# Kernel optimization log

Hardware: AMD Instinct MI355X
Metric: run time of the kernel (lower is better)

Reference implementation:

```python
import jax, jax.numpy as jnp
import numpy as np
from math import factorial

IRREPS = [0] * 256 + [1] * 256 + [2] * 128 + [3] * 64
N_BATCH, CHANNELS = 1024, 32


def _dfact(n):
    r = 1
    while n > 1:
        r *= n
        n -= 2
    return r


def _sh_l(l, xyz):
    """Real spherical harmonics of degree l, components m=-l..l, at unit vectors xyz."""
    x, y, z = xyz[:, 0], xyz[:, 1], xyz[:, 2]
    phi = np.arctan2(y, x)
    ct = z
    st = np.sqrt(np.clip(1.0 - ct * ct, 0.0, None))
    Y = np.zeros((xyz.shape[0], 2 * l + 1))
    for m in range(l + 1):
        pmm = ((-1.0) ** m) * _dfact(2 * m - 1) * st ** m  # P_m^m(cos t)
        if l == m:
            plm = pmm
        else:
            pm1 = ct * (2 * m + 1) * pmm  # P_{m+1}^m
            if l == m + 1:
                plm = pm1
            else:
                p2, p1 = pmm, pm1
                for ll in range(m + 2, l + 1):
                    p2, p1 = p1, ((2 * ll - 1) * ct * p1 - (ll + m - 1) * p2) / (ll - m)
                plm = p1
        K = np.sqrt((2 * l + 1) / (4 * np.pi) * factorial(l - m) / factorial(l + m))
        if m == 0:
            Y[:, l] = K * plm
        else:
            Y[:, l + m] = np.sqrt(2.0) * K * np.cos(m * phi) * plm
            Y[:, l - m] = np.sqrt(2.0) * K * np.sin(m * phi) * plm
    return Y


def _j_matrix(l):
    """Orthogonal involution J_l: real-SH matrix of the y<->z axis swap (J = J^T = J^-1)."""
    rng = np.random.default_rng(0)
    v = rng.normal(size=(max(256, 16 * (2 * l + 1)), 3))
    v /= np.linalg.norm(v, axis=1, keepdims=True)
    A = _sh_l(l, v)
    B = _sh_l(l, v[:, [0, 2, 1]])  # Y(swap r)
    X, _, _, _ = np.linalg.lstsq(A, B, rcond=None)
    return X.T  # Y(swap r) = J @ Y(r)


def _build_info():
    freq, rev, groups = [], [], []
    off = 0
    i = 0
    while i < len(IRREPS):
        l = IRREPS[i]
        mul = 0
        while i < len(IRREPS) and IRREPS[i] == l:
            mul += 1
            i += 1
        d = 2 * l + 1
        groups.append((l, off, mul, np.asarray(_j_matrix(l), np.float32)))
        for _ in range(mul):
            for k in range(d):
                freq.append(k - l)      # m value of component k
                rev.append(off + (d - 1 - k))  # index of the -m partner
            off += d
    return np.asarray(freq, np.float32), np.asarray(rev, np.int32), groups, off


FREQ_NP, REV_NP, GROUPS, DIM = _build_info()
FREQ = jnp.asarray(FREQ_NP)
REV = jnp.asarray(REV_NP)
J_MATS = [jnp.asarray(J) for (_, _, _, J) in GROUPS]


def _z_rot(x, theta):
    """Per-m z-rotation (sparse vecsca): out_m = cos(m t) x_m - sin(m t) x_{-m}."""
    ang = theta[:, None] * FREQ  # (N, DIM)
    return jnp.cos(ang)[..., None] * x - jnp.sin(ang)[..., None] * x[:, REV, :]


def _j_apply(x):
    """Block-diagonal J application, grouped by l (sparse scale / flip stage)."""
    n, _, c = x.shape
    outs = []
    for (l, off, mul, _), J in zip(GROUPS, J_MATS):
        d = 2 * l + 1
        seg = x[:, off:off + mul * d, :].reshape(n, mul, d, c)
        outs.append(jnp.einsum('pq,nmqc->nmpc', J, seg).reshape(n, mul * d, c))
    return jnp.concatenate(outs, axis=1)


def setup_inputs() -> dict:
    key = jax.random.key(0)
    k0, k1, k2, k3 = jax.random.split(key, 4)
    two_pi = 2.0 * np.pi
    return {
        'input': jax.random.normal(k0, (N_BATCH, DIM, CHANNELS), dtype=jnp.float32),
        'alpha': jax.random.uniform(k1, (N_BATCH,), dtype=jnp.float32) * two_pi,
        'beta': jax.random.uniform(k2, (N_BATCH,), dtype=jnp.float32) * two_pi,
        'gamma': jax.random.uniform(k3, (N_BATCH,), dtype=jnp.float32) * two_pi,
    }


def reference(input, alpha, beta, gamma):
    # D(alpha, beta, gamma) = Dz(alpha) J Dz(beta) J Dz(gamma)
    x = _z_rot(input, gamma)
    x = _j_apply(x)
    x = _z_rot(x, beta)
    x = _j_apply(x)
    return _z_rot(x, alpha)
```

## Files before the change

kernel.cpp:

```cpp
#include <hip/hip_runtime.h>
#include <math.h>


namespace {

constexpr float SQ3_2 = 0.86602540378443864676f;
constexpr float S6    = 0.61237243569579452455f;
constexpr float S10   = 0.79056941504209483300f;
constexpr float S15   = 0.96824583655185422129f;

template<int L> struct JM;
template<> struct JM<1> {
  static constexpr float v[3][3] = {
    { 0.f, -1.f, 0.f},
    {-1.f,  0.f, 0.f},
    { 0.f,  0.f, 1.f}};
};
template<> struct JM<2> {
  static constexpr float v[5][5] = {
    { 0.f, 0.f,  0.f,   -1.f,  0.f},
    { 0.f, 1.f,  0.f,    0.f,  0.f},
    { 0.f, 0.f, -0.5f,   0.f, -SQ3_2},
    {-1.f, 0.f,  0.f,    0.f,  0.f},
    { 0.f, 0.f, -SQ3_2,  0.f,  0.5f}};
};
template<> struct JM<3> {
  static constexpr float v[7][7] = {
    { 0.f, 0.f, 0.f, S10,  0.f,   -S6,  0.f},
    { 0.f, 1.f, 0.f, 0.f,  0.f,    0.f, 0.f},
    { 0.f, 0.f, 0.f, S6,   0.f,    S10, 0.f},
    { S10, 0.f, S6,  0.f,  0.f,    0.f, 0.f},
    { 0.f, 0.f, 0.f, 0.f, -0.25f,  0.f, -S15},
    {-S6,  0.f, S10, 0.f,  0.f,    0.f, 0.f},
    { 0.f, 0.f, 0.f, 0.f, -S15,    0.f, 0.25f}};
};

template<int L>
__device__ inline void compute_M_col(int q, float al, float be, float ga, float* M) {
  constexpr int D = 2 * L + 1;
  const int mq = q - L;
  float sg, cg;
  sincosf((float)mq * ga, &sg, &cg);
  float v[D];
#pragma unroll
  for (int p = 0; p < D; ++p)
    v[p] = cg * JM<L>::v[p][q] + sg * JM<L>::v[p][(D - 1) - q];
  float c1, s1;
  sincosf(be, &s1, &c1);
  float cb[L + 1], sb[L + 1];
  cb[0] = 1.f; sb[0] = 0.f;
  cb[1] = c1;  sb[1] = s1;
#pragma unroll
  for (int k = 2; k <= L; ++k) {
    cb[k] = 2.f * c1 * cb[k - 1] - cb[k - 2];
    sb[k] = 2.f * c1 * sb[k - 1] - sb[k - 2];
  }
  float w[D];
#pragma unroll
  for (int p = 0; p < D; ++p) {
    const int mp = p - L;
    const int am = mp < 0 ? -mp : mp;
    const float c = cb[am];
    const float s = mp < 0 ? -sb[am] : sb[am];
    w[p] = c * v[p] - s * v[(D - 1) - p];
  }
  float u[D];
#pragma unroll
  for (int p = 0; p < D; ++p) {
    float acc = 0.f;
#pragma unroll
    for (int r = 0; r < D; ++r) acc = fmaf(JM<L>::v[p][r], w[r], acc);
    u[p] = acc;
  }
  sincosf(al, &s1, &c1);
  float ca[L + 1], sa[L + 1];
  ca[0] = 1.f; sa[0] = 0.f;
  ca[1] = c1;  sa[1] = s1;
#pragma unroll
  for (int k = 2; k <= L; ++k) {
    ca[k] = 2.f * c1 * ca[k - 1] - ca[k - 2];
    sa[k] = 2.f * c1 * sa[k - 1] - sa[k - 2];
  }
#pragma unroll
  for (int p = 0; p < D; ++p) {
    const int mp = p - L;
    const int am = mp < 0 ? -mp : mp;
    const float c = ca[am];
    const float s = mp < 0 ? -sa[am] : sa[am];
    M[p * D + q] = c * u[p] - s * u[(D - 1) - p];
  }
}

template<int D>
__device__ inline void apply_block(const float4* __restrict__ inN,
                                   float4* __restrict__ outN,
                                   const float* __restrict__ M, int off, int ch) {
  float4 v[D];
#pragma unroll
  for (int q = 0; q < D; ++q) v[q] = inN[(off + q) * 8 + ch];
#pragma unroll
  for (int p = 0; p < D; ++p) {
    float m = M[p * D];
    float4 a;
    a.x = m * v[0].x; a.y = m * v[0].y; a.z = m * v[0].z; a.w = m * v[0].w;
#pragma unroll
    for (int q = 1; q < D; ++q) {
      m = M[p * D + q];
      a.x = fmaf(m, v[q].x, a.x);
      a.y = fmaf(m, v[q].y, a.y);
      a.z = fmaf(m, v[q].z, a.z);
      a.w = fmaf(m, v[q].w, a.w);
    }
    outN[(off + p) * 8 + ch] = a;
  }
}

__global__ __launch_bounds__(256) void wigner_d_kernel(
    const float* __restrict__ in, const float* __restrict__ alpha,
    const float* __restrict__ beta, const float* __restrict__ gamma,
    float* __restrict__ out) {
  __shared__ float M1[9], M2[25], M3[49];
  const int n = blockIdx.x;
  const int t = threadIdx.x;

  if (t < 19) {
    const float al = alpha[n], be = beta[n], ga = gamma[n];
    if (t < 7)                  compute_M_col<3>(t,      al, be, ga, M3);
    else if (t >= 8 && t < 13)  compute_M_col<2>(t - 8,  al, be, ga, M2);
    else if (t >= 16)           compute_M_col<1>(t - 16, al, be, ga, M1);
  }
  __syncthreads();

  const size_t base = (size_t)n * (2112 * 8);
  const float4* inN = (const float4*)in + base;
  float4* outN = (float4*)out + base;
  const int g = t >> 3;
  const int ch = t & 7;

#pragma unroll
  for (int j = 0; j < 8; ++j) {
    const int r = 32 * j + g;
    outN[r * 8 + ch] = inN[r * 8 + ch];
  }
  for (int j = 0; j < 8; ++j)
    apply_block<3>(inN, outN, M1, 256 + 3 * (32 * j + g), ch);
  for (int j = 0; j < 4; ++j)
    apply_block<5>(inN, outN, M2, 1024 + 5 * (32 * j + g), ch);
  for (int j = 0; j < 2; ++j)
    apply_block<7>(inN, outN, M3, 1664 + 7 * (32 * j + g), ch);
}

}

extern "C" void kernel_launch(void* const* d_in, const int* in_sizes, int n_in,
                              void* d_out, int out_size, void* d_ws, size_t ws_size,
                              hipStream_t stream) {
  const float* in    = (const float*)d_in[0];
  const float* alpha = (const float*)d_in[1];
  const float* beta  = (const float*)d_in[2];
  const float* gamma = (const float*)d_in[3];
  float* out = (float*)d_out;
  const int n_batch = in_sizes[1];
  wigner_d_kernel<<<n_batch, 256, 0, stream>>>(in, alpha, beta, gamma, out);
}
```

Before: 115.9 us.

## Precompute Wigner matrices in separate kernel, widen blocks, use nontemporal IO

Moves the per-sample Wigner D matrix construction into a separate small kernel that writes to workspace. The streaming kernel then only loads the 83 coefficients into shared memory, so the serial trig prologue no longer stalls the whole block. Blocks grow to 512 threads with fully unrolled loops, and all global loads and stores use nontemporal hints. The cost is an extra kernel launch plus a workspace round trip, and a fused fallback is kept for when the workspace is too small.

```diff
diff --git a/kernel.cpp b/kernel.cpp
--- a/kernel.cpp
+++ b/kernel.cpp
@@ -3,6 +3,8 @@
 
 
 namespace {
+
+typedef float f4 __attribute__((ext_vector_type(4)));
 
 constexpr float SQ3_2 = 0.86602540378443864676f;
 constexpr float S6    = 0.61237243569579452455f;
@@ -91,63 +93,91 @@
   }
 }
 
+__global__ __launch_bounds__(256) void build_M_kernel(
+    const float* __restrict__ alpha, const float* __restrict__ beta,
+    const float* __restrict__ gamma, float* __restrict__ ws, int n_batch) {
+  const int t = threadIdx.x;
+  const int n = blockIdx.x * 16 + (t >> 4);
+  const int col = t & 15;
+  if (n >= n_batch || col >= 15) return;
+  const float al = alpha[n], be = beta[n], ga = gamma[n];
+  float* w = ws + (size_t)n * 96;
+  if (col < 7)       compute_M_col<3>(col,      al, be, ga, w);
+  else if (col < 12) compute_M_col<2>(col - 7,  al, be, ga, w + 49);
+  else               compute_M_col<1>(col - 12, al, be, ga, w + 74);
+}
+
 template<int D>
-__device__ inline void apply_block(const float4* __restrict__ inN,
-                                   float4* __restrict__ outN,
+__device__ inline void apply_block(const f4* __restrict__ inN,
+                                   f4* __restrict__ outN,
                                    const float* __restrict__ M, int off, int ch) {
-  float4 v[D];
-#pragma unroll
-  for (int q = 0; q < D; ++q) v[q] = inN[(off + q) * 8 + ch];
-#pragma unroll
-  for (int p = 0; p < D; ++p) {
-    float m = M[p * D];
-    float4 a;
-    a.x = m * v[0].x; a.y = m * v[0].y; a.z = m * v[0].z; a.w = m * v[0].w;
-#pragma unroll
-    for (int q = 1; q < D; ++q) {
-      m = M[p * D + q];
-      a.x = fmaf(m, v[q].x, a.x);
-      a.y = fmaf(m, v[q].y, a.y);
-      a.z = fmaf(m, v[q].z, a.z);
-      a.w = fmaf(m, v[q].w, a.w);
-    }
-    outN[(off + p) * 8 + ch] = a;
-  }
-}
-
-__global__ __launch_bounds__(256) void wigner_d_kernel(
+  f4 v[D];
+#pragma unroll
+  for (int q = 0; q < D; ++q)
+    v[q] = __builtin_nontemporal_load(&inN[(off + q) * 8 + ch]);
+#pragma unroll
+  for (int p = 0; p < D; ++p) {
+    f4 a = M[p * D] * v[0];
+#pragma unroll
+    for (int q = 1; q < D; ++q) a += M[p * D + q] * v[q];
+    __builtin_nontemporal_store(a, &outN[(off + p) * 8 + ch]);
+  }
+}
+
+__device__ inline void stream_body(const float* __restrict__ in,
+                                   float* __restrict__ out,
+                                   const float* __restrict__ M,
+                                   int n, int t) {
+  const float* M3 = M;
+  const float* M2 = M + 49;
+  const float* M1 = M + 74;
+  const size_t base = (size_t)n * (2112 * 8);
+  const f4* inN = (const f4*)in + base;
+  f4* outN = (f4*)out + base;
+  const int g = t >> 3;
+  const int ch = t & 7;
+
+#pragma unroll
+  for (int j = 0; j < 4; ++j) {
+    const int r = 64 * j + g;
+    __builtin_nontemporal_store(__builtin_nontemporal_load(&inN[r * 8 + ch]),
+                                &outN[r * 8 + ch]);
+  }
+#pragma unroll
+  for (int j = 0; j < 4; ++j)
+    apply_block<3>(inN, outN, M1, 256 + 3 * (64 * j + g), ch);
+#pragma unroll
+  for (int j = 0; j < 2; ++j)
+    apply_block<5>(inN, outN, M2, 1024 + 5 * (64 * j + g), ch);
+  apply_block<7>(inN, outN, M3, 1664 + 7 * g, ch);
+}
+
+__global__ __launch_bounds__(512, 8) void wigner_stream_kernel(
+    const float* __restrict__ in, const float* __restrict__ ws,
+    float* __restrict__ out) {
+  __shared__ float M[96];
+  const int n = blockIdx.x;
+  const int t = threadIdx.x;
+  if (t < 83) M[t] = ws[(size_t)n * 96 + t];
+  __syncthreads();
+  stream_body(in, out, M, n, t);
+}
+
+__global__ __launch_bounds__(512) void wigner_fused_kernel(
     const float* __restrict__ in, const float* __restrict__ alpha,
     const float* __restrict__ beta, const float* __restrict__ gamma,
     float* __restrict__ out) {
-  __shared__ float M1[9], M2[25], M3[49];
+  __shared__ float M[96];
   const int n = blockIdx.x;
   const int t = threadIdx.x;
-
-  if (t < 19) {
+  if (t < 15) {
     const float al = alpha[n], be = beta[n], ga = gamma[n];
-    if (t < 7)                  compute_M_col<3>(t,      al, be, ga, M3);
-    else if (t >= 8 && t < 13)  compute_M_col<2>(t - 8,  al, be, ga, M2);
-    else if (t >= 16)           compute_M_col<1>(t - 16, al, be, ga, M1);
+    if (t < 7)       compute_M_col<3>(t,      al, be, ga, M);
+    else if (t < 12) compute_M_col<2>(t - 7,  al, be, ga, M + 49);
+    else             compute_M_col<1>(t - 12, al, be, ga, M + 74);
   }
   __syncthreads();
-
-  const size_t base = (size_t)n * (2112 * 8);
-  const float4* inN = (const float4*)in + base;
-  float4* outN = (float4*)out + base;
-  const int g = t >> 3;
-  const int ch = t & 7;
-
-#pragma unroll
-  for (int j = 0; j < 8; ++j) {
-    const int r = 32 * j + g;
-    outN[r * 8 + ch] = inN[r * 8 + ch];
-  }
-  for (int j = 0; j < 8; ++j)
-    apply_block<3>(inN, outN, M1, 256 + 3 * (32 * j + g), ch);
-  for (int j = 0; j < 4; ++j)
-    apply_block<5>(inN, outN, M2, 1024 + 5 * (32 * j + g), ch);
-  for (int j = 0; j < 2; ++j)
-    apply_block<7>(inN, outN, M3, 1664 + 7 * (32 * j + g), ch);
+  stream_body(in, out, M, n, t);
 }
 
 }
@@ -161,5 +191,14 @@
   const float* gamma = (const float*)d_in[3];
   float* out = (float*)d_out;
   const int n_batch = in_sizes[1];
-  wigner_d_kernel<<<n_batch, 256, 0, stream>>>(in, alpha, beta, gamma, out);
-}
+
+  const size_t ws_needed = (size_t)n_batch * 96 * sizeof(float);
+  if (ws_size >= ws_needed) {
+    float* ws = (float*)d_ws;
+    build_M_kernel<<<(n_batch + 15) / 16, 256, 0, stream>>>(alpha, beta, gamma,
+                                                            ws, n_batch);
+    wigner_stream_kernel<<<n_batch, 512, 0, stream>>>(in, ws, out);
+  } else {
+    wigner_fused_kernel<<<n_batch, 512, 0, stream>>>(in, alpha, beta, gamma, out);
+  }
+}
```

Measured after the change: 117.0 us. No clear change (+0.9%).
